# Kernel tuning notes

Measured on AMD Instinct MI355X. Metric: run time of the kernel, lower is better.

Reference implementation:

```python
import jax, jax.numpy as jnp
import numpy as np

MARGIN = 6.0
EPSILON = 2.0
REL_DIM = 256
REL_RANGE = (MARGIN + EPSILON) / REL_DIM  # OpenKE rel_embedding_range = 0.03125
PI = 3.14159265358979323846


def setup_inputs() -> dict:
    key = jax.random.key(0)
    k1, k2, k3, k4, k5 = jax.random.split(key, 5)
    B, S, H = 16, 64, 768
    E, D2 = 43234, 512  # entity count, entity embed dim (2*256)
    return {
        "question_hidden": jax.random.normal(k1, (B, S, H), dtype=jnp.float32),
        "W_rel": jax.random.normal(k2, (18, H), dtype=jnp.float32) * 0.02,
        "b_rel": jnp.zeros((18,), dtype=jnp.float32),
        "rel_embeddings": jax.random.normal(k3, (18, REL_DIM), dtype=jnp.float32) * REL_RANGE,
        "ent_embeddings": jax.random.normal(k4, (E, D2), dtype=jnp.float32) * 0.05,
        "head_id": jax.random.randint(k5, (B,), 0, E, dtype=jnp.int64),
    }


def reference(question_hidden, W_rel, b_rel, rel_embeddings, ent_embeddings, head_id):
    # RelationPredictor: mean-pool BERT hidden states, then Linear(768 -> 18)
    q = jnp.mean(question_hidden, axis=1)                       # (B, 768)
    rel_scores = q @ W_rel.T + b_rel                            # (B, 18)
    # soft relation mixture -> predicted relation embedding
    predict_relation = jax.nn.sigmoid(rel_scores) @ rel_embeddings  # (B, 256)
    head = ent_embeddings[head_id]                              # (B, 512)
    re_h, im_h = jnp.split(head, 2, axis=-1)                    # (B, 256) each
    phase = predict_relation / (REL_RANGE / PI)
    re_r, im_r = jnp.cos(phase), jnp.sin(phase)
    # rotate head by relation (complex multiply)
    rot_re = re_h * re_r - im_h * im_r                          # (B, 256)
    rot_im = re_h * im_r + im_h * re_r                          # (B, 256)
    re_t, im_t = jnp.split(ent_embeddings, 2, axis=-1)          # (E, 256) each
    # broadcast distance vs all entities: (B, E, 256) intermediates
    dre = rot_re[:, None, :] - re_t[None, :, :]
    dim_ = rot_im[:, None, :] - im_t[None, :, :]
    dist = jnp.sqrt(dre * dre + dim_ * dim_).sum(axis=-1)       # (B, E)
    return MARGIN - dist
```

## Files before the change

### kernel.cpp

```cpp
#include <hip/hip_runtime.h>
#include <hip/hip_bf16.h>
#include <math.h>

#define MARGIN_F 6.0f
#define PHASE_SCALE 100.53096491487338f

__global__ void k_prep(const float* __restrict__ qh, const float* __restrict__ W,
                       const float* __restrict__ brel,
                       const float* __restrict__ rel,
                       const float* __restrict__ ent, const int* __restrict__ hid,
                       float* __restrict__ rot) {
    __shared__ float q[768];
    __shared__ float sig[18];
    int b = blockIdx.x;
    int t = threadIdx.x;

    if (t < 768) {
        float s = 0.f;
        const float* base = qh + (size_t)b * 64 * 768 + t;
        #pragma unroll 8
        for (int srow = 0; srow < 64; ++srow) s += base[(size_t)srow * 768];
        q[t] = s * (1.0f / 64.0f);
    }
    __syncthreads();

    int wave = t >> 6, lane = t & 63;
    for (int r = wave; r < 18; r += 16) {
        float p = 0.f;
        for (int h = lane; h < 768; h += 64) p += q[h] * W[r * 768 + h];
        for (int off = 32; off; off >>= 1) p += __shfl_xor(p, off, 64);
        if (lane == 0) sig[r] = 1.0f / (1.0f + expf(-(p + brel[r])));
    }
    __syncthreads();

    if (t < 256) {
        int d = t;
        float pr = 0.f;
        #pragma unroll
        for (int r = 0; r < 18; ++r) pr += sig[r] * rel[r * 256 + d];
        float phase = pr * PHASE_SCALE;
        float sn, cs;
        sincosf(phase, &sn, &cs);
        int h0 = hid[b];
        float reh = ent[(size_t)h0 * 512 + d];
        float imh = ent[(size_t)h0 * 512 + 256 + d];
        rot[b * 256 + d]        = reh * cs - imh * sn;
        rot[4096 + b * 256 + d] = reh * sn + imh * cs;
    }
}

__global__ __launch_bounds__(256, 4) void k_dist(const float* __restrict__ ent,
                                                 const float* __restrict__ rot,
                                                 float* __restrict__ out, int E,
                                                 int chunk) {
    int lane = threadIdx.x & 63;
    int w4 = threadIdx.x >> 6;

    const float4* rre4 = (const float4*)rot + (size_t)w4 * 4 * 64;
    const float4* rim4 = (const float4*)(rot + 4096) + (size_t)w4 * 4 * 64;
    float4 ra[4], ia[4];
    #pragma unroll
    for (int b = 0; b < 4; ++b) {
        ra[b] = rre4[b * 64 + lane];
        ia[b] = rim4[b * 64 + lane];
    }
    #pragma unroll
    for (int b = 0; b < 4; ++b) {
        asm volatile("" : "+v"(ra[b].x), "+v"(ra[b].y), "+v"(ra[b].z), "+v"(ra[b].w));
        asm volatile("" : "+v"(ia[b].x), "+v"(ia[b].y), "+v"(ia[b].z), "+v"(ia[b].w));
    }

    int bout = w4 * 4 + (((lane & 1) << 1) | ((lane >> 1) & 1));

    int e0 = blockIdx.x * chunk;
    int e1 = min(e0 + chunk, E);

    for (int e = e0; e < e1; e += 2) {
        int ea = e;
        int eb = min(e + 1, e1 - 1);
        const float4* r4a = (const float4*)(ent + (size_t)ea * 512);
        const float4* r4b = (const float4*)(ent + (size_t)eb * 512);
        float4 tea = r4a[lane], tia = r4a[64 + lane];
        float4 teb = r4b[lane], tib = r4b[64 + lane];

        float va[4], vb[4];
        #pragma unroll
        for (int b = 0; b < 4; ++b) {
            float dx0 = ra[b].x - tea.x, dy0 = ia[b].x - tia.x;
            float dx1 = ra[b].y - tea.y, dy1 = ia[b].y - tia.y;
            float dx2 = ra[b].z - tea.z, dy2 = ia[b].z - tia.z;
            float dx3 = ra[b].w - tea.w, dy3 = ia[b].w - tia.w;
            float s0 = __builtin_amdgcn_sqrtf(dx0 * dx0 + dy0 * dy0);
            float s1 = __builtin_amdgcn_sqrtf(dx1 * dx1 + dy1 * dy1);
            float s2 = __builtin_amdgcn_sqrtf(dx2 * dx2 + dy2 * dy2);
            float s3 = __builtin_amdgcn_sqrtf(dx3 * dx3 + dy3 * dy3);
            va[b] = (s0 + s1) + (s2 + s3);

            float ex0 = ra[b].x - teb.x, ey0 = ia[b].x - tib.x;
            float ex1 = ra[b].y - teb.y, ey1 = ia[b].y - tib.y;
            float ex2 = ra[b].z - teb.z, ey2 = ia[b].z - tib.z;
            float ex3 = ra[b].w - teb.w, ey3 = ia[b].w - tib.w;
            float u0 = __builtin_amdgcn_sqrtf(ex0 * ex0 + ey0 * ey0);
            float u1 = __builtin_amdgcn_sqrtf(ex1 * ex1 + ey1 * ey1);
            float u2 = __builtin_amdgcn_sqrtf(ex2 * ex2 + ey2 * ey2);
            float u3 = __builtin_amdgcn_sqrtf(ex3 * ex3 + ey3 * ey3);
            vb[b] = (u0 + u1) + (u2 + u3);
        }

        #pragma unroll
        for (int i = 0; i < 2; ++i) {
            float sa = (lane & 1) ? va[i] : va[i + 2];
            float sb = (lane & 1) ? vb[i] : vb[i + 2];
            float ca = __shfl_xor(sa, 1, 64);
            float cb = __shfl_xor(sb, 1, 64);
            va[i] = ((lane & 1) ? va[i + 2] : va[i]) + ca;
            vb[i] = ((lane & 1) ? vb[i + 2] : vb[i]) + cb;
        }
        {
            float sa = (lane & 2) ? va[0] : va[1];
            float sb = (lane & 2) ? vb[0] : vb[1];
            float ca = __shfl_xor(sa, 2, 64);
            float cb = __shfl_xor(sb, 2, 64);
            va[0] = ((lane & 2) ? va[1] : va[0]) + ca;
            vb[0] = ((lane & 2) ? vb[1] : vb[0]) + cb;
        }
        va[0] += __shfl_xor(va[0], 4, 64);
        vb[0] += __shfl_xor(vb[0], 4, 64);
        va[0] += __shfl_xor(va[0], 8, 64);
        vb[0] += __shfl_xor(vb[0], 8, 64);
        va[0] += __shfl_xor(va[0], 16, 64);
        vb[0] += __shfl_xor(vb[0], 16, 64);
        va[0] += __shfl_xor(va[0], 32, 64);
        vb[0] += __shfl_xor(vb[0], 32, 64);

        if (lane < 4) {
            out[(size_t)bout * E + ea] = MARGIN_F - va[0];
            if (e + 1 < e1) out[(size_t)bout * E + e + 1] = MARGIN_F - vb[0];
        }
    }
}

extern "C" void kernel_launch(void* const* d_in, const int* in_sizes, int n_in,
                              void* d_out, int out_size, void* d_ws,
                              size_t ws_size, hipStream_t stream) {
    const float* qh   = (const float*)d_in[0];
    const float* W    = (const float*)d_in[1];
    const float* brel = (const float*)d_in[2];
    const float* rel  = (const float*)d_in[3];
    const float* ent  = (const float*)d_in[4];
    const int*   hid  = (const int*)d_in[5];
    float* out = (float*)d_out;

    int E = in_sizes[4] / 512;

    float* rot = (float*)d_ws;

    k_prep<<<dim3(16), 1024, 0, stream>>>(qh, W, brel, rel, ent, hid, rot);

    const int NB = 2048;
    int chunk = (E + NB - 1) / NB;
    k_dist<<<dim3(NB), 256, 0, stream>>>(ent, rot, out, E, chunk);
}
```

Before: 58.80 us.

## Stage entity rows through LDS with register-prefetched double buffering

Entity rows for the distance kernel now go through shared memory. Each block cooperatively loads 8 rows, which each of its four waves previously fetched from global memory on its own. The next group is prefetched into registers while the current one is computed, then written to LDS between barriers. This is meant to cut redundant global or L2 traffic and hide load latency, at the cost of two block-wide barriers per group plus extra LDS use and register pressure.

```diff
diff --git a/kernel.cpp b/kernel.cpp
--- a/kernel.cpp
+++ b/kernel.cpp
@@ -49,12 +49,17 @@
     }
 }
 
+#define PH 8
+
 __global__ __launch_bounds__(256, 4) void k_dist(const float* __restrict__ ent,
                                                  const float* __restrict__ rot,
                                                  float* __restrict__ out, int E,
                                                  int chunk) {
-    int lane = threadIdx.x & 63;
-    int w4 = threadIdx.x >> 6;
+    __shared__ float4 buf[PH * 128];
+
+    int t = threadIdx.x;
+    int lane = t & 63;
+    int w4 = t >> 6;
 
     const float4* rre4 = (const float4*)rot + (size_t)w4 * 4 * 64;
     const float4* rim4 = (const float4*)(rot + 4096) + (size_t)w4 * 4 * 64;
@@ -73,70 +78,106 @@
     int bout = w4 * 4 + (((lane & 1) << 1) | ((lane >> 1) & 1));
 
     int e0 = blockIdx.x * chunk;
+    if (e0 >= E) return;
     int e1 = min(e0 + chunk, E);
-
-    for (int e = e0; e < e1; e += 2) {
-        int ea = e;
-        int eb = min(e + 1, e1 - 1);
-        const float4* r4a = (const float4*)(ent + (size_t)ea * 512);
-        const float4* r4b = (const float4*)(ent + (size_t)eb * 512);
-        float4 tea = r4a[lane], tia = r4a[64 + lane];
-        float4 teb = r4b[lane], tib = r4b[64 + lane];
-
-        float va[4], vb[4];
+    int nph = (e1 - e0 + PH - 1) / PH;
+
+    float4 sr[4];
+    #pragma unroll
+    for (int p = 0; p < 4; ++p) {
+        int slot = p * 256 + t;
+        int row = slot >> 7, j = slot & 127;
+        int er = min(e0 + row, E - 1);
+        sr[p] = ((const float4*)(ent + (size_t)er * 512))[j];
+    }
+    #pragma unroll
+    for (int p = 0; p < 4; ++p) buf[p * 256 + t] = sr[p];
+    __syncthreads();
+
+    for (int ph = 0; ph < nph; ++ph) {
+        int ebase = e0 + ph * PH;
+        bool more = (ph + 1) < nph;
+        if (more) {
+            int nbase = ebase + PH;
+            #pragma unroll
+            for (int p = 0; p < 4; ++p) {
+                int slot = p * 256 + t;
+                int row = slot >> 7, j = slot & 127;
+                int er = min(nbase + row, E - 1);
+                sr[p] = ((const float4*)(ent + (size_t)er * 512))[j];
+            }
+        }
+
         #pragma unroll
-        for (int b = 0; b < 4; ++b) {
-            float dx0 = ra[b].x - tea.x, dy0 = ia[b].x - tia.x;
-            float dx1 = ra[b].y - tea.y, dy1 = ia[b].y - tia.y;
-            float dx2 = ra[b].z - tea.z, dy2 = ia[b].z - tia.z;
-            float dx3 = ra[b].w - tea.w, dy3 = ia[b].w - tia.w;
-            float s0 = __builtin_amdgcn_sqrtf(dx0 * dx0 + dy0 * dy0);
-            float s1 = __builtin_amdgcn_sqrtf(dx1 * dx1 + dy1 * dy1);
-            float s2 = __builtin_amdgcn_sqrtf(dx2 * dx2 + dy2 * dy2);
-            float s3 = __builtin_amdgcn_sqrtf(dx3 * dx3 + dy3 * dy3);
-            va[b] = (s0 + s1) + (s2 + s3);
-
-            float ex0 = ra[b].x - teb.x, ey0 = ia[b].x - tib.x;
-            float ex1 = ra[b].y - teb.y, ey1 = ia[b].y - tib.y;
-            float ex2 = ra[b].z - teb.z, ey2 = ia[b].z - tib.z;
-            float ex3 = ra[b].w - teb.w, ey3 = ia[b].w - tib.w;
-            float u0 = __builtin_amdgcn_sqrtf(ex0 * ex0 + ey0 * ey0);
-            float u1 = __builtin_amdgcn_sqrtf(ex1 * ex1 + ey1 * ey1);
-            float u2 = __builtin_amdgcn_sqrtf(ex2 * ex2 + ey2 * ey2);
-            float u3 = __builtin_amdgcn_sqrtf(ex3 * ex3 + ey3 * ey3);
-            vb[b] = (u0 + u1) + (u2 + u3);
+        for (int g = 0; g < PH; g += 2) {
+            float4 tea = buf[g * 128 + lane];
+            float4 tia = buf[g * 128 + 64 + lane];
+            float4 teb = buf[(g + 1) * 128 + lane];
+            float4 tib = buf[(g + 1) * 128 + 64 + lane];
+
+            float va[4], vb[4];
+            #pragma unroll
+            for (int b = 0; b < 4; ++b) {
+                float dx0 = ra[b].x - tea.x, dy0 = ia[b].x - tia.x;
+                float dx1 = ra[b].y - tea.y, dy1 = ia[b].y - tia.y;
+                float dx2 = ra[b].z - tea.z, dy2 = ia[b].z - tia.z;
+                float dx3 = ra[b].w - tea.w, dy3 = ia[b].w - tia.w;
+                float s0 = __builtin_amdgcn_sqrtf(dx0 * dx0 + dy0 * dy0);
+                float s1 = __builtin_amdgcn_sqrtf(dx1 * dx1 + dy1 * dy1);
+                float s2 = __builtin_amdgcn_sqrtf(dx2 * dx2 + dy2 * dy2);
+                float s3 = __builtin_amdgcn_sqrtf(dx3 * dx3 + dy3 * dy3);
+                va[b] = (s0 + s1) + (s2 + s3);
+
+                float ex0 = ra[b].x - teb.x, ey0 = ia[b].x - tib.x;
+                float ex1 = ra[b].y - teb.y, ey1 = ia[b].y - tib.y;
+                float ex2 = ra[b].z - teb.z, ey2 = ia[b].z - tib.z;
+                float ex3 = ra[b].w - teb.w, ey3 = ia[b].w - tib.w;
+                float u0 = __builtin_amdgcn_sqrtf(ex0 * ex0 + ey0 * ey0);
+                float u1 = __builtin_amdgcn_sqrtf(ex1 * ex1 + ey1 * ey1);
+                float u2 = __builtin_amdgcn_sqrtf(ex2 * ex2 + ey2 * ey2);
+                float u3 = __builtin_amdgcn_sqrtf(ex3 * ex3 + ey3 * ey3);
+                vb[b] = (u0 + u1) + (u2 + u3);
+            }
+
+            #pragma unroll
+            for (int i = 0; i < 2; ++i) {
+                float sa = (lane & 1) ? va[i] : va[i + 2];
+                float sb = (lane & 1) ? vb[i] : vb[i + 2];
+                float ca = __shfl_xor(sa, 1, 64);
+                float cb = __shfl_xor(sb, 1, 64);
+                va[i] = ((lane & 1) ? va[i + 2] : va[i]) + ca;
+                vb[i] = ((lane & 1) ? vb[i + 2] : vb[i]) + cb;
+            }
+            {
+                float sa = (lane & 2) ? va[0] : va[1];
+                float sb = (lane & 2) ? vb[0] : vb[1];
+                float ca = __shfl_xor(sa, 2, 64);
+                float cb = __shfl_xor(sb, 2, 64);
+                va[0] = ((lane & 2) ? va[1] : va[0]) + ca;
+                vb[0] = ((lane & 2) ? vb[1] : vb[0]) + cb;
+            }
+            va[0] += __shfl_xor(va[0], 4, 64);
+            vb[0] += __shfl_xor(vb[0], 4, 64);
+            va[0] += __shfl_xor(va[0], 8, 64);
+            vb[0] += __shfl_xor(vb[0], 8, 64);
+            va[0] += __shfl_xor(va[0], 16, 64);
+            vb[0] += __shfl_xor(vb[0], 16, 64);
+            va[0] += __shfl_xor(va[0], 32, 64);
+            vb[0] += __shfl_xor(vb[0], 32, 64);
+
+            if (lane < 4) {
+                int eg = ebase + g;
+                if (eg < e1) out[(size_t)bout * E + eg] = MARGIN_F - va[0];
+                if (eg + 1 < e1) out[(size_t)bout * E + eg + 1] = MARGIN_F - vb[0];
+            }
         }
 
-        #pragma unroll
-        for (int i = 0; i < 2; ++i) {
-            float sa = (lane & 1) ? va[i] : va[i + 2];
-            float sb = (lane & 1) ? vb[i] : vb[i + 2];
-            float ca = __shfl_xor(sa, 1, 64);
-            float cb = __shfl_xor(sb, 1, 64);
-            va[i] = ((lane & 1) ? va[i + 2] : va[i]) + ca;
-            vb[i] = ((lane & 1) ? vb[i + 2] : vb[i]) + cb;
+        __syncthreads();
+        if (more) {
+            #pragma unroll
+            for (int p = 0; p < 4; ++p) buf[p * 256 + t] = sr[p];
         }
-        {
-            float sa = (lane & 2) ? va[0] : va[1];
-            float sb = (lane & 2) ? vb[0] : vb[1];
-            float ca = __shfl_xor(sa, 2, 64);
-            float cb = __shfl_xor(sb, 2, 64);
-            va[0] = ((lane & 2) ? va[1] : va[0]) + ca;
-            vb[0] = ((lane & 2) ? vb[1] : vb[0]) + cb;
-        }
-        va[0] += __shfl_xor(va[0], 4, 64);
-        vb[0] += __shfl_xor(vb[0], 4, 64);
-        va[0] += __shfl_xor(va[0], 8, 64);
-        vb[0] += __shfl_xor(vb[0], 8, 64);
-        va[0] += __shfl_xor(va[0], 16, 64);
-        vb[0] += __shfl_xor(vb[0], 16, 64);
-        va[0] += __shfl_xor(va[0], 32, 64);
-        vb[0] += __shfl_xor(vb[0], 32, 64);
-
-        if (lane < 4) {
-            out[(size_t)bout * E + ea] = MARGIN_F - va[0];
-            if (e + 1 < e1) out[(size_t)bout * E + e + 1] = MARGIN_F - vb[0];
-        }
+        __syncthreads();
     }
 }
 
```

After: 73.07 us. 1.24x slower.

## Double-buffer entity rows in LDS via async global_load_lds prefetch

Applied to the files above, without the earlier changes.

Each block now stages 8 entity rows at a time into a double-buffered shared-memory array using direct global-to-LDS loads, prefetching the next phase while the current one is computed. Before this, every wave read the same entity rows straight from global memory, so the four waves issued redundant loads. The aim is to share each row across waves and overlap the loads with the sqrt math. In exchange it adds a block barrier per phase and extra LDS traffic, and it relies on the async load completing before the barrier without an explicit vmcnt wait.

```diff
diff --git a/kernel.cpp b/kernel.cpp
--- a/kernel.cpp
+++ b/kernel.cpp
@@ -49,12 +49,17 @@
     }
 }
 
+#define PH 8
+
 __global__ __launch_bounds__(256, 4) void k_dist(const float* __restrict__ ent,
                                                  const float* __restrict__ rot,
                                                  float* __restrict__ out, int E,
                                                  int chunk) {
-    int lane = threadIdx.x & 63;
-    int w4 = threadIdx.x >> 6;
+    __shared__ float4 buf[2][PH * 128];
+
+    int t = threadIdx.x;
+    int lane = t & 63;
+    int w4 = t >> 6;
 
     const float4* rre4 = (const float4*)rot + (size_t)w4 * 4 * 64;
     const float4* rim4 = (const float4*)(rot + 4096) + (size_t)w4 * 4 * 64;
@@ -73,70 +78,101 @@
     int bout = w4 * 4 + (((lane & 1) << 1) | ((lane >> 1) & 1));
 
     int e0 = blockIdx.x * chunk;
+    if (e0 >= E) return;
     int e1 = min(e0 + chunk, E);
+    int nph = (e1 - e0 + PH - 1) / PH;
 
-    for (int e = e0; e < e1; e += 2) {
-        int ea = e;
-        int eb = min(e + 1, e1 - 1);
-        const float4* r4a = (const float4*)(ent + (size_t)ea * 512);
-        const float4* r4b = (const float4*)(ent + (size_t)eb * 512);
-        float4 tea = r4a[lane], tia = r4a[64 + lane];
-        float4 teb = r4b[lane], tib = r4b[64 + lane];
-
-        float va[4], vb[4];
-        #pragma unroll
-        for (int b = 0; b < 4; ++b) {
-            float dx0 = ra[b].x - tea.x, dy0 = ia[b].x - tia.x;
-            float dx1 = ra[b].y - tea.y, dy1 = ia[b].y - tia.y;
-            float dx2 = ra[b].z - tea.z, dy2 = ia[b].z - tia.z;
-            float dx3 = ra[b].w - tea.w, dy3 = ia[b].w - tia.w;
-            float s0 = __builtin_amdgcn_sqrtf(dx0 * dx0 + dy0 * dy0);
-            float s1 = __builtin_amdgcn_sqrtf(dx1 * dx1 + dy1 * dy1);
-            float s2 = __builtin_amdgcn_sqrtf(dx2 * dx2 + dy2 * dy2);
-            float s3 = __builtin_amdgcn_sqrtf(dx3 * dx3 + dy3 * dy3);
-            va[b] = (s0 + s1) + (s2 + s3);
-
-            float ex0 = ra[b].x - teb.x, ey0 = ia[b].x - tib.x;
-            float ex1 = ra[b].y - teb.y, ey1 = ia[b].y - tib.y;
-            float ex2 = ra[b].z - teb.z, ey2 = ia[b].z - tib.z;
-            float ex3 = ra[b].w - teb.w, ey3 = ia[b].w - tib.w;
-            float u0 = __builtin_amdgcn_sqrtf(ex0 * ex0 + ey0 * ey0);
-            float u1 = __builtin_amdgcn_sqrtf(ex1 * ex1 + ey1 * ey1);
-            float u2 = __builtin_amdgcn_sqrtf(ex2 * ex2 + ey2 * ey2);
-            float u3 = __builtin_amdgcn_sqrtf(ex3 * ex3 + ey3 * ey3);
-            vb[b] = (u0 + u1) + (u2 + u3);
+    #define STAGE(bi, ebase)                                                     \
+        {                                                                        \
+            _Pragma("unroll") for (int p = 0; p < 4; ++p) {                      \
+                int slotbase = p * 256 + w4 * 64;                                \
+                int row = slotbase >> 7;                                         \
+                int jbase = slotbase & 127;                                      \
+                int er = min((ebase) + row, E - 1);                              \
+                const float* src =                                               \
+                    ent + (size_t)er * 512 + (size_t)(jbase + lane) * 4;         \
+                __builtin_amdgcn_global_load_lds(                                \
+                    (const __attribute__((address_space(1))) void*)src,          \
+                    (__attribute__((address_space(3))) void*)&buf[bi][slotbase], \
+                    16, 0, 0);                                                   \
+            }                                                                    \
         }
 
+    STAGE(0, e0);
+    __syncthreads();
+
+    int cur = 0;
+    for (int ph = 0; ph < nph; ++ph) {
+        int ebase = e0 + ph * PH;
+        if (ph + 1 < nph) STAGE(cur ^ 1, ebase + PH);
+
+        const float4* B = buf[cur];
         #pragma unroll
-        for (int i = 0; i < 2; ++i) {
-            float sa = (lane & 1) ? va[i] : va[i + 2];
-            float sb = (lane & 1) ? vb[i] : vb[i + 2];
-            float ca = __shfl_xor(sa, 1, 64);
-            float cb = __shfl_xor(sb, 1, 64);
-            va[i] = ((lane & 1) ? va[i + 2] : va[i]) + ca;
-            vb[i] = ((lane & 1) ? vb[i + 2] : vb[i]) + cb;
+        for (int g = 0; g < PH; g += 2) {
+            float4 tea = B[g * 128 + lane];
+            float4 tia = B[g * 128 + 64 + lane];
+            float4 teb = B[(g + 1) * 128 + lane];
+            float4 tib = B[(g + 1) * 128 + 64 + lane];
+
+            float va[4], vb[4];
+            #pragma unroll
+            for (int b = 0; b < 4; ++b) {
+                float dx0 = ra[b].x - tea.x, dy0 = ia[b].x - tia.x;
+                float dx1 = ra[b].y - tea.y, dy1 = ia[b].y - tia.y;
+                float dx2 = ra[b].z - tea.z, dy2 = ia[b].z - tia.z;
+                float dx3 = ra[b].w - tea.w, dy3 = ia[b].w - tia.w;
+                float s0 = __builtin_amdgcn_sqrtf(dx0 * dx0 + dy0 * dy0);
+                float s1 = __builtin_amdgcn_sqrtf(dx1 * dx1 + dy1 * dy1);
+                float s2 = __builtin_amdgcn_sqrtf(dx2 * dx2 + dy2 * dy2);
+                float s3 = __builtin_amdgcn_sqrtf(dx3 * dx3 + dy3 * dy3);
+                va[b] = (s0 + s1) + (s2 + s3);
+
+                float ex0 = ra[b].x - teb.x, ey0 = ia[b].x - tib.x;
+                float ex1 = ra[b].y - teb.y, ey1 = ia[b].y - tib.y;
+                float ex2 = ra[b].z - teb.z, ey2 = ia[b].z - tib.z;
+                float ex3 = ra[b].w - teb.w, ey3 = ia[b].w - tib.w;
+                float u0 = __builtin_amdgcn_sqrtf(ex0 * ex0 + ey0 * ey0);
+                float u1 = __builtin_amdgcn_sqrtf(ex1 * ex1 + ey1 * ey1);
+                float u2 = __builtin_amdgcn_sqrtf(ex2 * ex2 + ey2 * ey2);
+                float u3 = __builtin_amdgcn_sqrtf(ex3 * ex3 + ey3 * ey3);
+                vb[b] = (u0 + u1) + (u2 + u3);
+            }
+
+            #pragma unroll
+            for (int i = 0; i < 2; ++i) {
+                float sa = (lane & 1) ? va[i] : va[i + 2];
+                float sb = (lane & 1) ? vb[i] : vb[i + 2];
+                float ca = __shfl_xor(sa, 1, 64);
+                float cb = __shfl_xor(sb, 1, 64);
+                va[i] = ((lane & 1) ? va[i + 2] : va[i]) + ca;
+                vb[i] = ((lane & 1) ? vb[i + 2] : vb[i]) + cb;
+            }
+            {
+                float sa = (lane & 2) ? va[0] : va[1];
+                float sb = (lane & 2) ? vb[0] : vb[1];
+                float ca = __shfl_xor(sa, 2, 64);
+                float cb = __shfl_xor(sb, 2, 64);
+                va[0] = ((lane & 2) ? va[1] : va[0]) + ca;
+                vb[0] = ((lane & 2) ? vb[1] : vb[0]) + cb;
+            }
+            va[0] += __shfl_xor(va[0], 4, 64);
+            vb[0] += __shfl_xor(vb[0], 4, 64);
+            va[0] += __shfl_xor(va[0], 8, 64);
+            vb[0] += __shfl_xor(vb[0], 8, 64);
+            va[0] += __shfl_xor(va[0], 16, 64);
+            vb[0] += __shfl_xor(vb[0], 16, 64);
+            va[0] += __shfl_xor(va[0], 32, 64);
+            vb[0] += __shfl_xor(vb[0], 32, 64);
+
+            if (lane < 4) {
+                int eg = ebase + g;
+                if (eg < e1) out[(size_t)bout * E + eg] = MARGIN_F - va[0];
+                if (eg + 1 < e1) out[(size_t)bout * E + eg + 1] = MARGIN_F - vb[0];
+            }
         }
-        {
-            float sa = (lane & 2) ? va[0] : va[1];
-            float sb = (lane & 2) ? vb[0] : vb[1];
-            float ca = __shfl_xor(sa, 2, 64);
-            float cb = __shfl_xor(sb, 2, 64);
-            va[0] = ((lane & 2) ? va[1] : va[0]) + ca;
-            vb[0] = ((lane & 2) ? vb[1] : vb[0]) + cb;
-        }
-        va[0] += __shfl_xor(va[0], 4, 64);
-        vb[0] += __shfl_xor(vb[0], 4, 64);
-        va[0] += __shfl_xor(va[0], 8, 64);
-        vb[0] += __shfl_xor(vb[0], 8, 64);
-        va[0] += __shfl_xor(va[0], 16, 64);
-        vb[0] += __shfl_xor(vb[0], 16, 64);
-        va[0] += __shfl_xor(va[0], 32, 64);
-        vb[0] += __shfl_xor(vb[0], 32, 64);
 
-        if (lane < 4) {
-            out[(size_t)bout * E + ea] = MARGIN_F - va[0];
-            if (e + 1 < e1) out[(size_t)bout * E + e + 1] = MARGIN_F - vb[0];
-        }
+        __syncthreads();
+        cur ^= 1;
     }
 }
 
```

Result: slower. 65.81 us (+11.9%).
